# Performance work log

Hardware: AMD Instinct MI355X
Metric: run time of the kernel (lower is better)

The kernel has to match this reference:

```python
import jax, jax.numpy as jnp
import numpy as np

# dims
B, N, D, H, S, LT, DE = 16, 32, 64, 8, 8, 128, 256  # B scenes, N trajs, d_in, heads, splits, seq, d_expand
L = LT // S
GROUPS = 8
EPS = 1e-5


def group_norm(x, gamma, beta):
    # x: (BN, C, L); normalize per group over (C//G, L)
    BN, C, Lx = x.shape
    xg = x.reshape(BN, GROUPS, (C // GROUPS) * Lx)
    mu = xg.mean(-1, keepdims=True)
    var = xg.var(-1, keepdims=True)
    xn = ((xg - mu) * jax.lax.rsqrt(var + EPS)).reshape(BN, C, Lx)
    return xn * gamma[None, :, None] + beta[None, :, None]


def conv1d(x, w, b, pad):
    # x: (BN, Cin, L), w: (Cout, Cin, K)
    y = jax.lax.conv_general_dilated(x, w, (1,), [(pad, pad)],
                                     dimension_numbers=('NCH', 'OIH', 'NCH'))
    return y + b[None, :, None]


def setup_inputs() -> dict:
    key = jax.random.key(0)
    ks = jax.random.split(key, 8)
    d_qkv = 3 * H * D
    sc = 0.02
    return {
        'x': jax.random.normal(ks[0], (B * N, D, LT), jnp.float32),
        'gn1_g': jnp.ones((D,), jnp.float32),
        'gn1_b': jnp.zeros((D,), jnp.float32),
        'w_qkv': sc * jax.random.normal(ks[1], (d_qkv, D, 3), jnp.float32),
        'b_qkv': jnp.zeros((d_qkv,), jnp.float32),
        'w_merge': sc * jax.random.normal(ks[2], (D, H * D, 3), jnp.float32),
        'b_merge': jnp.zeros((D,), jnp.float32),
        'gn2_g': jnp.ones((D,), jnp.float32),
        'gn2_b': jnp.zeros((D,), jnp.float32),
        'w_ff1': sc * jax.random.normal(ks[3], (DE, D, 3), jnp.float32),
        'b_ff1': jnp.zeros((DE,), jnp.float32),
        'w_ff2': sc * jax.random.normal(ks[4], (D, DE, 3), jnp.float32),
        'b_ff2': jnp.zeros((D,), jnp.float32),
    }


def reference(x, gn1_g, gn1_b, w_qkv, b_qkv, w_merge, b_merge,
              gn2_g, gn2_b, w_ff1, b_ff1, w_ff2, b_ff2):
    # QKV projection: GroupNorm + Conv1d(k=3,p=1)
    qkv = conv1d(group_norm(x, gn1_g, gn1_b), w_qkv, b_qkv, 1)  # (B*N, 3*H*D, LT)
    # rearrange '(B N) (T H C) (L S) -> T (B H) (N S) (C L)'
    qkv = qkv.reshape(B, N, 3, H, D, L, S).transpose(2, 0, 3, 1, 6, 4, 5)
    qkv = qkv.reshape(3, B * H, N * S, D * L)
    q, k, v = qkv[0], qkv[1], qkv[2]
    # attn = 1 / cdist(q, k, p=2)  (dropout is identity in eval mode)
    sq = ((q * q).sum(-1)[:, :, None] + (k * k).sum(-1)[:, None, :]
          - 2.0 * jnp.einsum('bid,bjd->bij', q, k))
    dist = jnp.sqrt(jnp.maximum(sq, 1e-12))
    attn = 1.0 / dist
    out = jnp.einsum('bij,bjd->bid', attn, v)  # (B*H, N*S, D*L)
    # rearrange '(B H) (N S) (C L) -> (B N) (H C) (L S)'
    out = out.reshape(B, H, N, S, D, L).transpose(0, 2, 1, 4, 5, 3)
    out = out.reshape(B * N, H * D, LT)
    x = x + conv1d(out, w_merge, b_merge, 1)
    # FFN: GroupNorm -> Conv -> Swish -> Conv ; shortcut is Identity (d_in==d_out)
    h = conv1d(group_norm(x, gn2_g, gn2_b), w_ff1, b_ff1, 1)
    h = h * jax.nn.sigmoid(h)
    y = conv1d(h, w_ff2, b_ff2, 1)
    return y + x
```

## Files before the change

kernel.cpp:

```cpp
#include <hip/hip_runtime.h>
#include <hip/hip_bf16.h>

#define DEV __device__ __forceinline__

typedef __attribute__((ext_vector_type(8))) __bf16 bf16x8;
typedef __attribute__((ext_vector_type(4))) float f32x4;

DEV float bfu(unsigned short u) { return __uint_as_float((unsigned int)u << 16); }
DEV unsigned short f2bf(float f) {
    union { float f; unsigned int u; } cv; cv.f = f;
    unsigned int u = cv.u;
    unsigned int r = (u + 0x7fffu + ((u >> 16) & 1u)) >> 16;
    return (unsigned short)r;
}
DEV unsigned int pack2(float a, float b) {
    return (unsigned int)f2bf(a) | ((unsigned int)f2bf(b) << 16);
}


__global__ __launch_bounds__(256) void gnstats_kernel(const float* __restrict__ src,
    const float* __restrict__ gamma, const float* __restrict__ beta,
    float* __restrict__ sa, float* __restrict__ sb)
{
    __shared__ float gsum[8], gsq[8];
    const int s = blockIdx.x, tid = threadIdx.x;
    const int g = tid >> 5, il = tid & 31;
    const float* p = src + (size_t)s * 8192 + g * 1024 + il;
    float sm = 0.f, sq = 0.f;
    #pragma unroll
    for (int m = 0; m < 32; ++m) {
        float v = p[m * 32];
        sm += v; sq += v * v;
    }
    #pragma unroll
    for (int m = 16; m; m >>= 1) { sm += __shfl_xor(sm, m); sq += __shfl_xor(sq, m); }
    if (il == 0) { gsum[g] = sm; gsq[g] = sq; }
    __syncthreads();
    if (tid < 64) {
        int gg = tid >> 3;
        float mu = gsum[gg] * (1.f / 1024.f);
        float var = gsq[gg] * (1.f / 1024.f) - mu * mu;
        float a = gamma[tid] * rsqrtf(var + 1e-5f);
        sa[s * 64 + tid] = a;
        sb[s * 64 + tid] = beta[tid] - mu * a;
    }
}

__global__ __launch_bounds__(256) void xprep_kernel(const float* __restrict__ src,
    const float* __restrict__ sa, const float* __restrict__ sb,
    unsigned short* __restrict__ xnt)
{
    __shared__ __align__(16) float sx[64][133];
    __shared__ float la[64], lb[64];
    const int s = blockIdx.x, tid = threadIdx.x;
    if (tid < 64) { la[tid] = sa[s * 64 + tid]; lb[tid] = sb[s * 64 + tid]; }
    for (int idx = tid; idx < 8192; idx += 256) {
        int c = idx >> 7, lt = idx & 127;
        sx[c][lt] = src[(size_t)s * 8192 + idx];
    }
    __syncthreads();
    for (int idx = tid; idx < 8320; idx += 256) {
        int row = idx >> 6, c = idx & 63;
        float v = 0.f;
        if (row >= 1 && row <= 128) v = sx[c][row - 1] * la[c] + lb[c];
        xnt[(size_t)s * 8320 + idx] = f2bf(v);
    }
}

__global__ __launch_bounds__(256) void prep_w_kernel(const float* __restrict__ w,
    unsigned short* __restrict__ dst, int n)
{
    int i = blockIdx.x * 256 + threadIdx.x;
    if (i < n) {
        #pragma unroll
        for (int k = 0; k < 3; ++k)
            dst[k * n + i] = f2bf(w[(size_t)i * 3 + k]);
    }
}

__global__ __launch_bounds__(256, 3) void conv_qkv_mfma(
    const unsigned short* __restrict__ xnt,
    const unsigned short* __restrict__ wq, const float* __restrict__ bias,
    unsigned short* __restrict__ qb, unsigned short* __restrict__ kb,
    unsigned short* __restrict__ vb, float* __restrict__ nq, float* __restrict__ nk,
    int b0)
{
    __shared__ __align__(16) char smem[34816];
    unsigned short (*xt)[72]  = (unsigned short(*)[72])smem;
    unsigned short (*ct)[136] = (unsigned short(*)[136])smem;

    const int mc = blockIdx.x, sl = blockIdx.y, tid = threadIdx.x;
    const int bn = b0 * 32 + sl;
    const int w = tid >> 6, lane = tid & 63;
    const int lrow = lane & 15, lko = (lane >> 4) * 8, q4 = lane >> 4;

    bf16x8 af[3][2][2];
    #pragma unroll
    for (int k = 0; k < 3; ++k)
        #pragma unroll
        for (int kc = 0; kc < 2; ++kc)
            #pragma unroll
            for (int m = 0; m < 2; ++m)
                af[k][kc][m] = *(const bf16x8*)(wq + (size_t)k * 98304 +
                    (size_t)(mc * 128 + w * 32 + m * 16 + lrow) * 64 + kc * 32 + lko);

    for (int idx = tid; idx < 1040; idx += 256)
        *(uint4*)&xt[idx >> 3][(idx & 7) * 8] = *(const uint4*)(xnt + (size_t)bn * 8320 + idx * 8);
    __syncthreads();

    f32x4 acc[2][8];
    #pragma unroll
    for (int m = 0; m < 2; ++m)
        #pragma unroll
        for (int n = 0; n < 8; ++n) acc[m][n] = (f32x4)0.f;
    #pragma unroll
    for (int k = 0; k < 3; ++k) {
        #pragma unroll
        for (int kc = 0; kc < 2; ++kc) {
            #pragma unroll
            for (int n = 0; n < 8; ++n) {
                bf16x8 b = *(const bf16x8*)&xt[n * 16 + lrow + k][kc * 32 + lko];
                acc[0][n] = __builtin_amdgcn_mfma_f32_16x16x32_bf16(af[k][kc][0], b, acc[0][n], 0, 0, 0);
                acc[1][n] = __builtin_amdgcn_mfma_f32_16x16x32_bf16(af[k][kc][1], b, acc[1][n], 0, 0, 0);
            }
        }
    }
    __syncthreads();
    const int c0 = mc * 128;
    float bv[2][4];
    #pragma unroll
    for (int m = 0; m < 2; ++m)
        #pragma unroll
        for (int r = 0; r < 4; ++r)
            bv[m][r] = bias[c0 + w * 32 + m * 16 + q4 * 4 + r];
    #pragma unroll
    for (int m = 0; m < 2; ++m)
        #pragma unroll
        for (int n = 0; n < 8; ++n)
            #pragma unroll
            for (int r = 0; r < 4; ++r)
                ct[w * 32 + m * 16 + q4 * 4 + r][n * 16 + lrow] =
                    f2bf(acc[m][n][r] + bv[m][r]);
    __syncthreads();
    const int t = mc >> 2, h_base = (mc & 3) * 2;
    const int bl = sl >> 5, n_tr = sl & 31;
    if (t < 2) {
        unsigned short* dst = t ? kb : qb;
        for (int idx = tid; idx < 2048; idx += 256) {
            int lb = idx & 1;
            int d  = (idx >> 1) & 63;
            int s  = (idx >> 7) & 7;
            int hl = idx >> 10;
            unsigned int uu[4];
            #pragma unroll
            for (int e2 = 0; e2 < 4; ++e2) {
                unsigned short w0 = ct[hl * 64 + d][(lb * 8 + e2 * 2) * 8 + s];
                unsigned short w1 = ct[hl * 64 + d][(lb * 8 + e2 * 2 + 1) * 8 + s];
                uu[e2] = (unsigned int)w0 | ((unsigned int)w1 << 16);
            }
            uint4 o = {uu[0], uu[1], uu[2], uu[3]};
            size_t a = ((size_t)((bl * 8 + h_base + hl) * 256 + n_tr * 8 + s)) * 1024 + d * 16 + lb * 8;
            *(uint4*)(dst + a) = o;
        }
        float* ndst = t ? nk : nq;
        const int tk = tid >> 4, l = tid & 15;
        const int hl = tk >> 3, sS = tk & 7;
        float s2 = 0.f;
        for (int d = 0; d < 64; ++d) {
            float v = bfu(ct[hl * 64 + d][l * 8 + sS]);
            s2 = fmaf(v, v, s2);
        }
        #pragma unroll
        for (int m = 8; m; m >>= 1) s2 += __shfl_xor(s2, m);
        if (l == 0)
            ndst[(bl * 8 + h_base + hl) * 256 + n_tr * 8 + sS] = s2;
    } else {
        for (int idx = tid; idx < 2048; idx += 256) {
            int l = idx & 15, d = (idx >> 4) & 63, hl = idx >> 10;
            uint4 o = *(const uint4*)&ct[hl * 64 + d][l * 8];
            size_t a = ((size_t)((bl * 8 + h_base + hl) * 1024 + d * 16 + l)) * 256 + n_tr * 8;
            *(uint4*)(vb + a) = o;
        }
    }
}

__global__ __launch_bounds__(256) void attnw_mfma(const unsigned short* __restrict__ qb,
    const unsigned short* __restrict__ kb, const float* __restrict__ nq,
    const float* __restrict__ nk, unsigned short* __restrict__ attn)
{
    __shared__ __align__(16) unsigned short q_s[128][136];
    __shared__ __align__(16) unsigned short k_s[128][136];
    const int bh = blockIdx.z, i0 = blockIdx.y * 128, j0 = blockIdx.x * 128;
    const int tid = threadIdx.x, w = tid >> 6, lane = tid & 63;
    const int wi = w >> 1, wj = w & 1;
    const int lrow = lane & 15, lko = (lane >> 4) * 8;
    f32x4 acc[4][4];
    #pragma unroll
    for (int m = 0; m < 4; ++m)
        #pragma unroll
        for (int n = 0; n < 4; ++n) acc[m][n] = (f32x4)0.f;
    const size_t tb = (size_t)bh * 262144;
    for (int fc = 0; fc < 8; ++fc) {
        __syncthreads();
        for (int idx = tid; idx < 2048; idx += 256) {
            int r = idx >> 4, c8 = (idx & 15) * 8;
            *(uint4*)&q_s[r][c8] = *(const uint4*)(qb + tb + (size_t)(i0 + r) * 1024 + fc * 128 + c8);
            *(uint4*)&k_s[r][c8] = *(const uint4*)(kb + tb + (size_t)(j0 + r) * 1024 + fc * 128 + c8);
        }
        __syncthreads();
        #pragma unroll
        for (int ks = 0; ks < 4; ++ks) {
            bf16x8 a[4], b[4];
            #pragma unroll
            for (int m = 0; m < 4; ++m) a[m] = *(const bf16x8*)&q_s[wi * 64 + m * 16 + lrow][ks * 32 + lko];
            #pragma unroll
            for (int n = 0; n < 4; ++n) b[n] = *(const bf16x8*)&k_s[wj * 64 + n * 16 + lrow][ks * 32 + lko];
            #pragma unroll
            for (int m = 0; m < 4; ++m)
                #pragma unroll
                for (int n = 0; n < 4; ++n)
                    acc[m][n] = __builtin_amdgcn_mfma_f32_16x16x32_bf16(a[m], b[n], acc[m][n], 0, 0, 0);
        }
    }
    float nqv[4][4], nkv[4];
    #pragma unroll
    for (int m = 0; m < 4; ++m)
        #pragma unroll
        for (int r = 0; r < 4; ++r)
            nqv[m][r] = nq[bh * 256 + i0 + wi * 64 + m * 16 + (lane >> 4) * 4 + r];
    #pragma unroll
    for (int n = 0; n < 4; ++n)
        nkv[n] = nk[bh * 256 + j0 + wj * 64 + n * 16 + lrow];
    __syncthreads();
    #pragma unroll
    for (int m = 0; m < 4; ++m)
        #pragma unroll
        for (int n = 0; n < 4; ++n)
            #pragma unroll
            for (int r = 0; r < 4; ++r) {
                float sq = nqv[m][r] + nkv[n] - 2.f * acc[m][n][r];
                q_s[wi * 64 + m * 16 + (lane >> 4) * 4 + r][wj * 64 + n * 16 + lrow] =
                    f2bf(rsqrtf(fmaxf(sq, 1e-12f)));
            }
    __syncthreads();
    for (int idx = tid; idx < 2048; idx += 256) {
        int r = idx >> 4, c8 = (idx & 15) * 8;
        *(uint4*)(attn + (size_t)bh * 65536 + (size_t)(i0 + r) * 256 + j0 + c8) =
            *(const uint4*)&q_s[r][c8];
    }
}

__global__ __launch_bounds__(256) void pv_mfma(const unsigned short* __restrict__ attn,
    const unsigned short* __restrict__ vb, unsigned short* __restrict__ umat)
{
    __shared__ __align__(16) unsigned short a_s[128][136];
    __shared__ __align__(16) unsigned short b_s[128][136];
    const int bh = blockIdx.z, i0 = blockIdx.y * 128, f0 = blockIdx.x * 128;
    const int tid = threadIdx.x, w = tid >> 6, lane = tid & 63;
    const int wi = w >> 1, wf = w & 1;
    const int lrow = lane & 15, lko = (lane >> 4) * 8;
    f32x4 acc[4][4];
    #pragma unroll
    for (int m = 0; m < 4; ++m)
        #pragma unroll
        for (int n = 0; n < 4; ++n) acc[m][n] = (f32x4)0.f;
    for (int jc = 0; jc < 2; ++jc) {
        __syncthreads();
        for (int idx = tid; idx < 2048; idx += 256) {
            int r = idx >> 4, c8 = (idx & 15) * 8;
            *(uint4*)&a_s[r][c8] = *(const uint4*)(attn + (size_t)bh * 65536 + (size_t)(i0 + r) * 256 + jc * 128 + c8);
            *(uint4*)&b_s[r][c8] = *(const uint4*)(vb + (size_t)bh * 262144 + (size_t)(f0 + r) * 256 + jc * 128 + c8);
        }
        __syncthreads();
        #pragma unroll
        for (int ks = 0; ks < 4; ++ks) {
            bf16x8 a[4], b[4];
            #pragma unroll
            for (int m = 0; m < 4; ++m) a[m] = *(const bf16x8*)&a_s[wi * 64 + m * 16 + lrow][ks * 32 + lko];
            #pragma unroll
            for (int n = 0; n < 4; ++n) b[n] = *(const bf16x8*)&b_s[wf * 64 + n * 16 + lrow][ks * 32 + lko];
            #pragma unroll
            for (int m = 0; m < 4; ++m)
                #pragma unroll
                for (int n = 0; n < 4; ++n)
                    acc[m][n] = __builtin_amdgcn_mfma_f32_16x16x32_bf16(a[m], b[n], acc[m][n], 0, 0, 0);
        }
    }
    __syncthreads();
    #pragma unroll
    for (int m = 0; m < 4; ++m)
        #pragma unroll
        for (int n = 0; n < 4; ++n)
            #pragma unroll
            for (int r = 0; r < 4; ++r)
                a_s[wi * 64 + m * 16 + (lane >> 4) * 4 + r][wf * 64 + n * 16 + lrow] = f2bf(acc[m][n][r]);
    __syncthreads();
    const int bl = bh >> 3, h = bh & 7;
    const int cinb = h * 64 + (f0 >> 4);
    for (int idx = tid; idx < 2048; idx += 256) {
        int r = idx >> 4;
        int l = idx & 15;
        int i = i0 + r;
        int nn = i >> 3, s = i & 7;
        int lt = l * 8 + s;
        unsigned int uu[4];
        #pragma unroll
        for (int e = 0; e < 4; ++e) {
            unsigned short w0 = a_s[r][(e * 2 + 0) * 16 + l];
            unsigned short w1 = a_s[r][(e * 2 + 1) * 16 + l];
            uu[e] = (unsigned int)w0 | ((unsigned int)w1 << 16);
        }
        uint4 o = {uu[0], uu[1], uu[2], uu[3]};
        *(uint4*)(umat + ((size_t)(bl * 32 + nn) * 128 + lt) * 512 + cinb) = o;
    }
}

__global__ __launch_bounds__(256, 3) void merge_mfma(const unsigned short* __restrict__ umat,
    const float* __restrict__ x, const unsigned short* __restrict__ wmg,
    const float* __restrict__ bias, float* __restrict__ x2, int b0)
{
    __shared__ __align__(16) unsigned short ut[130][136];
    const int sl = blockIdx.x, tid = threadIdx.x;
    const int bn = b0 * 32 + sl;
    const int w = tid >> 6, lane = tid & 63;
    const int lrow = lane & 15, lko = (lane >> 4) * 8, q4 = lane >> 4;
    if (tid < 128) { ut[0][tid] = 0; ut[129][tid] = 0; }
    f32x4 acc[2][4];
    #pragma unroll
    for (int m = 0; m < 2; ++m)
        #pragma unroll
        for (int n = 0; n < 4; ++n) acc[m][n] = (f32x4)0.f;
    for (int c4 = 0; c4 < 4; ++c4) {
        __syncthreads();
        for (int idx = tid; idx < 2048; idx += 256) {
            int lt = idx >> 4, ci8 = (idx & 15) * 8;
            *(uint4*)&ut[1 + lt][ci8] =
                *(const uint4*)(umat + ((size_t)sl * 128 + lt) * 512 + c4 * 128 + ci8);
        }
        bf16x8 af[3][4][2];
        #pragma unroll
        for (int k = 0; k < 3; ++k)
            #pragma unroll
            for (int kc = 0; kc < 4; ++kc)
                #pragma unroll
                for (int m = 0; m < 2; ++m)
                    af[k][kc][m] = *(const bf16x8*)(wmg + (size_t)k * 32768 +
                        (size_t)((w >> 1) * 32 + m * 16 + lrow) * 512 + c4 * 128 + kc * 32 + lko);
        __syncthreads();
        #pragma unroll
        for (int k = 0; k < 3; ++k) {
            #pragma unroll
            for (int kc = 0; kc < 4; ++kc) {
                bf16x8 b[4];
                #pragma unroll
                for (int n = 0; n < 4; ++n)
                    b[n] = *(const bf16x8*)&ut[(w & 1) * 64 + n * 16 + lrow + k][kc * 32 + lko];
                #pragma unroll
                for (int m = 0; m < 2; ++m)
                    #pragma unroll
                    for (int n = 0; n < 4; ++n)
                        acc[m][n] = __builtin_amdgcn_mfma_f32_16x16x32_bf16(af[k][kc][m], b[n], acc[m][n], 0, 0, 0);
            }
        }
    }
    #pragma unroll
    for (int m = 0; m < 2; ++m) {
        int cb = (w >> 1) * 32 + m * 16 + q4 * 4;
        float bv[4];
        #pragma unroll
        for (int r = 0; r < 4; ++r) bv[r] = bias[cb + r];
        #pragma unroll
        for (int n = 0; n < 4; ++n) {
            int lt = (w & 1) * 64 + n * 16 + lrow;
            #pragma unroll
            for (int r = 0; r < 4; ++r) {
                size_t a = (size_t)bn * 8192 + (size_t)(cb + r) * 128 + lt;
                x2[a] = acc[m][n][r] + bv[r] + x[a];
            }
        }
    }
}

__global__ __launch_bounds__(256, 3) void ff1_mfma(const unsigned short* __restrict__ xnt,
    const unsigned short* __restrict__ wf1, const float* __restrict__ bias,
    unsigned short* __restrict__ hb)
{
    __shared__ __align__(16) unsigned short xt[130][72];
    const int mc = blockIdx.x, bn = blockIdx.y, tid = threadIdx.x;
    const int w = tid >> 6, lane = tid & 63;
    const int lrow = lane & 15, lko = (lane >> 4) * 8, q4 = lane >> 4;
    bf16x8 af[3][2][2];
    #pragma unroll
    for (int k = 0; k < 3; ++k)
        #pragma unroll
        for (int kc = 0; kc < 2; ++kc)
            #pragma unroll
            for (int m = 0; m < 2; ++m)
                af[k][kc][m] = *(const bf16x8*)(wf1 + (size_t)k * 16384 +
                    (size_t)(mc * 128 + w * 32 + m * 16 + lrow) * 64 + kc * 32 + lko);
    for (int idx = tid; idx < 1040; idx += 256)
        *(uint4*)&xt[idx >> 3][(idx & 7) * 8] = *(const uint4*)(xnt + (size_t)bn * 8320 + idx * 8);
    __syncthreads();
    f32x4 acc[2][8];
    #pragma unroll
    for (int m = 0; m < 2; ++m)
        #pragma unroll
        for (int n = 0; n < 8; ++n) acc[m][n] = (f32x4)0.f;
    #pragma unroll
    for (int k = 0; k < 3; ++k) {
        #pragma unroll
        for (int kc = 0; kc < 2; ++kc) {
            #pragma unroll
            for (int n = 0; n < 8; ++n) {
                bf16x8 b = *(const bf16x8*)&xt[n * 16 + lrow + k][kc * 32 + lko];
                acc[0][n] = __builtin_amdgcn_mfma_f32_16x16x32_bf16(af[k][kc][0], b, acc[0][n], 0, 0, 0);
                acc[1][n] = __builtin_amdgcn_mfma_f32_16x16x32_bf16(af[k][kc][1], b, acc[1][n], 0, 0, 0);
            }
        }
    }
    #pragma unroll
    for (int m = 0; m < 2; ++m) {
        int rb = w * 32 + m * 16 + q4 * 4;
        float bv[4];
        #pragma unroll
        for (int r = 0; r < 4; ++r) bv[r] = bias[mc * 128 + rb + r];
        #pragma unroll
        for (int n = 0; n < 8; ++n) {
            int lt = n * 16 + lrow;
            float sws[4];
            #pragma unroll
            for (int r = 0; r < 4; ++r) {
                float t = acc[m][n][r] + bv[r];
                sws[r] = t / (1.f + __expf(-t));
            }
            uint2 o = {pack2(sws[0], sws[1]), pack2(sws[2], sws[3])};
            *(uint2*)(hb + (size_t)bn * 32768 + (size_t)lt * 256 + mc * 128 + rb) = o;
        }
    }
}

__global__ __launch_bounds__(256, 3) void ff2_mfma(const unsigned short* __restrict__ hb,
    const float* __restrict__ x2, const unsigned short* __restrict__ wf2,
    const float* __restrict__ bias, float* __restrict__ y)
{
    __shared__ __align__(16) unsigned short ut[130][136];
    const int bn = blockIdx.x, tid = threadIdx.x;
    const int w = tid >> 6, lane = tid & 63;
    const int lrow = lane & 15, lko = (lane >> 4) * 8, q4 = lane >> 4;
    if (tid < 128) { ut[0][tid] = 0; ut[129][tid] = 0; }
    f32x4 acc[2][4];
    #pragma unroll
    for (int m = 0; m < 2; ++m)
        #pragma unroll
        for (int n = 0; n < 4; ++n) acc[m][n] = (f32x4)0.f;
    for (int c2 = 0; c2 < 2; ++c2) {
        __syncthreads();
        for (int idx = tid; idx < 2048; idx += 256) {
            int lt = idx >> 4, ci8 = (idx & 15) * 8;
            *(uint4*)&ut[1 + lt][ci8] =
                *(const uint4*)(hb + (size_t)bn * 32768 + (size_t)lt * 256 + c2 * 128 + ci8);
        }
        bf16x8 af[3][4][2];
        #pragma unroll
        for (int k = 0; k < 3; ++k)
            #pragma unroll
            for (int kc = 0; kc < 4; ++kc)
                #pragma unroll
                for (int m = 0; m < 2; ++m)
                    af[k][kc][m] = *(const bf16x8*)(wf2 + (size_t)k * 16384 +
                        (size_t)((w >> 1) * 32 + m * 16 + lrow) * 256 + c2 * 128 + kc * 32 + lko);
        __syncthreads();
        #pragma unroll
        for (int k = 0; k < 3; ++k) {
            #pragma unroll
            for (int kc = 0; kc < 4; ++kc) {
                bf16x8 b[4];
                #pragma unroll
                for (int n = 0; n < 4; ++n)
                    b[n] = *(const bf16x8*)&ut[(w & 1) * 64 + n * 16 + lrow + k][kc * 32 + lko];
                #pragma unroll
                for (int m = 0; m < 2; ++m)
                    #pragma unroll
                    for (int n = 0; n < 4; ++n)
                        acc[m][n] = __builtin_amdgcn_mfma_f32_16x16x32_bf16(af[k][kc][m], b[n], acc[m][n], 0, 0, 0);
            }
        }
    }
    #pragma unroll
    for (int m = 0; m < 2; ++m) {
        int cb = (w >> 1) * 32 + m * 16 + q4 * 4;
        float bv[4];
        #pragma unroll
        for (int r = 0; r < 4; ++r) bv[r] = bias[cb + r];
        #pragma unroll
        for (int n = 0; n < 4; ++n) {
            int lt = (w & 1) * 64 + n * 16 + lrow;
            #pragma unroll
            for (int r = 0; r < 4; ++r) {
                size_t a = (size_t)bn * 8192 + (size_t)(cb + r) * 128 + lt;
                y[a] = acc[m][n][r] + bv[r] + x2[a];
            }
        }
    }
}

extern "C" void kernel_launch(void* const* d_in, const int* in_sizes, int n_in,
                              void* d_out, int out_size, void* d_ws, size_t ws_size,
                              hipStream_t stream) {
    (void)in_sizes; (void)n_in; (void)out_size;
    const float* x     = (const float*)d_in[0];
    const float* gn1_g = (const float*)d_in[1];
    const float* gn1_b = (const float*)d_in[2];
    const float* w_qkv = (const float*)d_in[3];
    const float* b_qkv = (const float*)d_in[4];
    const float* w_mg  = (const float*)d_in[5];
    const float* b_mg  = (const float*)d_in[6];
    const float* gn2_g = (const float*)d_in[7];
    const float* gn2_b = (const float*)d_in[8];
    const float* w_f1  = (const float*)d_in[9];
    const float* b_f1  = (const float*)d_in[10];
    const float* w_f2  = (const float*)d_in[11];
    const float* b_f2  = (const float*)d_in[12];
    float* y = (float*)d_out;

    char* ws = (char*)d_ws;
    const size_t OFF_SA1 = 0;
    const size_t OFF_SB1 = 131072;
    const size_t OFF_SA2 = 262144;
    const size_t OFF_SB2 = 393216;
    const size_t OFF_NQ  = 524288;
    const size_t OFF_NK  = 655360;
    const size_t OFF_WQ  = 786432;
    const size_t OFF_WMG = 1376256;
    const size_t OFF_WF1 = 1572864;
    const size_t OFF_WF2 = 1671168;
    const size_t OFF_X2  = 2097152;
    const size_t OFF_XNT = 18874368;
    const size_t OFF_CHUNK = 27394048;
    const size_t H_BYTES = 33554432;

    int CH = 1;
    {
        const int cands[5] = {16, 8, 4, 2, 1};
        for (int ci = 0; ci < 5; ++ci) {
            int c = cands[ci];
            size_t qsz = (size_t)c * 4194304;
            size_t asz = (size_t)c * 1048576;
            size_t body = 3 * qsz + asz;
            if (body < H_BYTES) body = H_BYTES;
            if (OFF_CHUNK + body <= ws_size) { CH = c; break; }
        }
    }
    const size_t QSZ = (size_t)CH * 4194304;
    const size_t OFF_Q    = OFF_CHUNK;
    const size_t OFF_K    = OFF_Q + QSZ;
    const size_t OFF_V    = OFF_K + QSZ;
    const size_t OFF_ATTN = OFF_V + QSZ;

    float* sa1 = (float*)(ws + OFF_SA1);
    float* sb1 = (float*)(ws + OFF_SB1);
    float* sa2 = (float*)(ws + OFF_SA2);
    float* sb2 = (float*)(ws + OFF_SB2);
    float* nqp = (float*)(ws + OFF_NQ);
    float* nkp = (float*)(ws + OFF_NK);
    unsigned short* wqb  = (unsigned short*)(ws + OFF_WQ);
    unsigned short* wmgb = (unsigned short*)(ws + OFF_WMG);
    unsigned short* wf1b = (unsigned short*)(ws + OFF_WF1);
    unsigned short* wf2b = (unsigned short*)(ws + OFF_WF2);
    float* x2  = (float*)(ws + OFF_X2);
    unsigned short* xnt  = (unsigned short*)(ws + OFF_XNT);
    unsigned short* qb   = (unsigned short*)(ws + OFF_Q);
    unsigned short* kb   = (unsigned short*)(ws + OFF_K);
    unsigned short* vbuf = (unsigned short*)(ws + OFF_V);
    unsigned short* attn = (unsigned short*)(ws + OFF_ATTN);
    unsigned short* umat = (unsigned short*)(ws + OFF_Q);
    unsigned short* hbuf = (unsigned short*)(ws + OFF_CHUNK);

    gnstats_kernel<<<512, 256, 0, stream>>>(x, gn1_g, gn1_b, sa1, sb1);
    xprep_kernel<<<512, 256, 0, stream>>>(x, sa1, sb1, xnt);
    prep_w_kernel<<<384, 256, 0, stream>>>(w_qkv, wqb, 98304);
    prep_w_kernel<<<128, 256, 0, stream>>>(w_mg,  wmgb, 32768);
    prep_w_kernel<<<64,  256, 0, stream>>>(w_f1,  wf1b, 16384);
    prep_w_kernel<<<64,  256, 0, stream>>>(w_f2,  wf2b, 16384);
    const int nch = 16 / CH;
    for (int cidx = 0; cidx < nch; ++cidx) {
        int b0 = cidx * CH;
        conv_qkv_mfma<<<dim3(12, CH * 32), 256, 0, stream>>>(xnt, wqb, b_qkv, qb, kb, vbuf, nqp, nkp, b0);
        attnw_mfma<<<dim3(2, 2, CH * 8), 256, 0, stream>>>(qb, kb, nqp, nkp, attn);
        pv_mfma<<<dim3(8, 2, CH * 8), 256, 0, stream>>>(attn, vbuf, umat);
        merge_mfma<<<CH * 32, 256, 0, stream>>>(umat, x, wmgb, b_mg, x2, b0);
    }
    gnstats_kernel<<<512, 256, 0, stream>>>(x2, gn2_g, gn2_b, sa2, sb2);
    xprep_kernel<<<512, 256, 0, stream>>>(x2, sa2, sb2, xnt);
    ff1_mfma<<<dim3(2, 512), 256, 0, stream>>>(xnt, wf1b, b_f1, hbuf);
    ff2_mfma<<<512, 256, 0, stream>>>(hbuf, x2, wf2b, b_f2, y);
}
```

Measured before the change: 329.4 us.

## Fuse attention weight and PV matmuls into one kernel, add V transpose pass

Replaces the separate attention-weight kernel and PV kernel with a single fused kernel. Each block computes a 128x256 inverse-distance tile kept in shared memory, then multiplies it by V directly, so the attention matrix never goes to global memory. V is now written in the Q/K layout by the conv kernel and transposed by a new vtrans kernel. The fused kernel uses about 134KB of shared memory and launches only 2 x CH*8 blocks, so parallelism and occupancy are much lower.

```diff
diff --git a/kernel.cpp b/kernel.cpp
--- a/kernel.cpp
+++ b/kernel.cpp
@@ -82,7 +82,7 @@
     const unsigned short* __restrict__ xnt,
     const unsigned short* __restrict__ wq, const float* __restrict__ bias,
     unsigned short* __restrict__ qb, unsigned short* __restrict__ kb,
-    unsigned short* __restrict__ vb, float* __restrict__ nq, float* __restrict__ nk,
+    unsigned short* __restrict__ vt, float* __restrict__ nq, float* __restrict__ nk,
     int b0)
 {
     __shared__ __align__(16) char smem[34816];
@@ -144,24 +144,24 @@
     __syncthreads();
     const int t = mc >> 2, h_base = (mc & 3) * 2;
     const int bl = sl >> 5, n_tr = sl & 31;
+    unsigned short* dst = (t == 0) ? qb : ((t == 1) ? kb : vt);
+    for (int idx = tid; idx < 2048; idx += 256) {
+        int lb = idx & 1;
+        int d  = (idx >> 1) & 63;
+        int s  = (idx >> 7) & 7;
+        int hl = idx >> 10;
+        unsigned int uu[4];
+        #pragma unroll
+        for (int e2 = 0; e2 < 4; ++e2) {
+            unsigned short w0 = ct[hl * 64 + d][(lb * 8 + e2 * 2) * 8 + s];
+            unsigned short w1 = ct[hl * 64 + d][(lb * 8 + e2 * 2 + 1) * 8 + s];
+            uu[e2] = (unsigned int)w0 | ((unsigned int)w1 << 16);
+        }
+        uint4 o = {uu[0], uu[1], uu[2], uu[3]};
+        size_t a = ((size_t)((bl * 8 + h_base + hl) * 256 + n_tr * 8 + s)) * 1024 + d * 16 + lb * 8;
+        *(uint4*)(dst + a) = o;
+    }
     if (t < 2) {
-        unsigned short* dst = t ? kb : qb;
-        for (int idx = tid; idx < 2048; idx += 256) {
-            int lb = idx & 1;
-            int d  = (idx >> 1) & 63;
-            int s  = (idx >> 7) & 7;
-            int hl = idx >> 10;
-            unsigned int uu[4];
-            #pragma unroll
-            for (int e2 = 0; e2 < 4; ++e2) {
-                unsigned short w0 = ct[hl * 64 + d][(lb * 8 + e2 * 2) * 8 + s];
-                unsigned short w1 = ct[hl * 64 + d][(lb * 8 + e2 * 2 + 1) * 8 + s];
-                uu[e2] = (unsigned int)w0 | ((unsigned int)w1 << 16);
-            }
-            uint4 o = {uu[0], uu[1], uu[2], uu[3]};
-            size_t a = ((size_t)((bl * 8 + h_base + hl) * 256 + n_tr * 8 + s)) * 1024 + d * 16 + lb * 8;
-            *(uint4*)(dst + a) = o;
-        }
         float* ndst = t ? nk : nq;
         const int tk = tid >> 4, l = tid & 15;
         const int hl = tk >> 3, sS = tk & 7;
@@ -174,144 +174,165 @@
         for (int m = 8; m; m >>= 1) s2 += __shfl_xor(s2, m);
         if (l == 0)
             ndst[(bl * 8 + h_base + hl) * 256 + n_tr * 8 + sS] = s2;
-    } else {
-        for (int idx = tid; idx < 2048; idx += 256) {
-            int l = idx & 15, d = (idx >> 4) & 63, hl = idx >> 10;
-            uint4 o = *(const uint4*)&ct[hl * 64 + d][l * 8];
-            size_t a = ((size_t)((bl * 8 + h_base + hl) * 1024 + d * 16 + l)) * 256 + n_tr * 8;
-            *(uint4*)(vb + a) = o;
-        }
-    }
-}
-
-__global__ __launch_bounds__(256) void attnw_mfma(const unsigned short* __restrict__ qb,
+    }
+}
+
+__global__ __launch_bounds__(256) void vtrans_kernel(const unsigned short* __restrict__ vt,
+    unsigned short* __restrict__ vf)
+{
+    __shared__ __align__(16) unsigned short t_s[64][72];
+    const int dt = blockIdx.x, nt = blockIdx.y, bh = blockIdx.z, tid = threadIdx.x;
+    const size_t tb = (size_t)bh * 262144;
+    for (int idx = tid; idx < 512; idx += 256) {
+        int ns_l = idx >> 3, c8 = idx & 7;
+        int col = c8 ^ (ns_l >> 3);
+        *(uint4*)&t_s[ns_l][col * 8] =
+            *(const uint4*)(vt + tb + (size_t)(nt * 64 + ns_l) * 1024 + dt * 64 + c8 * 8);
+    }
+    __syncthreads();
+    for (int idx = tid; idx < 512; idx += 256) {
+        int dl_l = idx >> 3, nsb = idx & 7;
+        unsigned int uu[4];
+        #pragma unroll
+        for (int e2 = 0; e2 < 4; ++e2) {
+            int ns0 = nsb * 8 + e2 * 2, ns1 = ns0 + 1;
+            int cb = (dl_l >> 3) ^ nsb;
+            unsigned short w0 = t_s[ns0][cb * 8 + (dl_l & 7)];
+            unsigned short w1 = t_s[ns1][cb * 8 + (dl_l & 7)];
+            uu[e2] = (unsigned int)w0 | ((unsigned int)w1 << 16);
+        }
+        uint4 o = {uu[0], uu[1], uu[2], uu[3]};
+        *(uint4*)(vf + tb + (size_t)(dt * 64 + dl_l) * 256 + nt * 64 + nsb * 8) = o;
+    }
+}
+
+__global__ __launch_bounds__(256, 1) void attn_fused(const unsigned short* __restrict__ qb,
     const unsigned short* __restrict__ kb, const float* __restrict__ nq,
-    const float* __restrict__ nk, unsigned short* __restrict__ attn)
-{
-    __shared__ __align__(16) unsigned short q_s[128][136];
-    __shared__ __align__(16) unsigned short k_s[128][136];
-    const int bh = blockIdx.z, i0 = blockIdx.y * 128, j0 = blockIdx.x * 128;
-    const int tid = threadIdx.x, w = tid >> 6, lane = tid & 63;
+    const float* __restrict__ nk, const unsigned short* __restrict__ vf,
+    unsigned short* __restrict__ umat)
+{
+    __shared__ __align__(16) char smem[137216];
+    unsigned short (*Wm)[264] = (unsigned short(*)[264])smem;
+    unsigned short (*q_s)[136] = (unsigned short(*)[136])(smem + 67584);
+    unsigned short (*k_s)[136] = q_s + 128;
+    unsigned short (*b_s)[136] = q_s;
+    unsigned short (*ct)[264]  = (unsigned short(*)[264])(smem + 67584);
+
+    const int i0 = blockIdx.x, bh = blockIdx.y, tid = threadIdx.x;
+    const int w = tid >> 6, lane = tid & 63;
+    const int lrow = lane & 15, lko = (lane >> 4) * 8, q4 = lane >> 4;
+    const size_t tb = (size_t)bh * 262144;
+
     const int wi = w >> 1, wj = w & 1;
-    const int lrow = lane & 15, lko = (lane >> 4) * 8;
-    f32x4 acc[4][4];
+    float nqv[4][4];
     #pragma unroll
     for (int m = 0; m < 4; ++m)
         #pragma unroll
-        for (int n = 0; n < 4; ++n) acc[m][n] = (f32x4)0.f;
-    const size_t tb = (size_t)bh * 262144;
-    for (int fc = 0; fc < 8; ++fc) {
+        for (int r = 0; r < 4; ++r)
+            nqv[m][r] = nq[bh * 256 + i0 * 128 + wi * 64 + m * 16 + q4 * 4 + r];
+    for (int jh = 0; jh < 2; ++jh) {
+        f32x4 acc[4][4];
+        #pragma unroll
+        for (int m = 0; m < 4; ++m)
+            #pragma unroll
+            for (int n = 0; n < 4; ++n) acc[m][n] = (f32x4)0.f;
+        for (int fc = 0; fc < 8; ++fc) {
+            __syncthreads();
+            for (int idx = tid; idx < 2048; idx += 256) {
+                int r = idx >> 4, c8 = (idx & 15) * 8;
+                *(uint4*)&q_s[r][c8] = *(const uint4*)(qb + tb + (size_t)(i0 * 128 + r) * 1024 + fc * 128 + c8);
+                *(uint4*)&k_s[r][c8] = *(const uint4*)(kb + tb + (size_t)(jh * 128 + r) * 1024 + fc * 128 + c8);
+            }
+            __syncthreads();
+            #pragma unroll
+            for (int ks = 0; ks < 4; ++ks) {
+                bf16x8 a[4], b[4];
+                #pragma unroll
+                for (int m = 0; m < 4; ++m) a[m] = *(const bf16x8*)&q_s[wi * 64 + m * 16 + lrow][ks * 32 + lko];
+                #pragma unroll
+                for (int n = 0; n < 4; ++n) b[n] = *(const bf16x8*)&k_s[wj * 64 + n * 16 + lrow][ks * 32 + lko];
+                #pragma unroll
+                for (int m = 0; m < 4; ++m)
+                    #pragma unroll
+                    for (int n = 0; n < 4; ++n)
+                        acc[m][n] = __builtin_amdgcn_mfma_f32_16x16x32_bf16(a[m], b[n], acc[m][n], 0, 0, 0);
+            }
+        }
+        float nkv[4];
+        #pragma unroll
+        for (int n = 0; n < 4; ++n)
+            nkv[n] = nk[bh * 256 + jh * 128 + wj * 64 + n * 16 + lrow];
+        #pragma unroll
+        for (int m = 0; m < 4; ++m)
+            #pragma unroll
+            for (int n = 0; n < 4; ++n)
+                #pragma unroll
+                for (int r = 0; r < 4; ++r) {
+                    float sq = nqv[m][r] + nkv[n] - 2.f * acc[m][n][r];
+                    Wm[wi * 64 + m * 16 + q4 * 4 + r][jh * 128 + wj * 64 + n * 16 + lrow] =
+                        f2bf(rsqrtf(fmaxf(sq, 1e-12f)));
+                }
+    }
+
+    const int wi2 = w >> 1, wf2 = w & 1;
+    const int bl = bh >> 3, h = bh & 7;
+    for (int ch = 0; ch < 4; ++ch) {
+        f32x4 acc2[4][8];
+        #pragma unroll
+        for (int m = 0; m < 4; ++m)
+            #pragma unroll
+            for (int n = 0; n < 8; ++n) acc2[m][n] = (f32x4)0.f;
+        for (int jc = 0; jc < 2; ++jc) {
+            __syncthreads();
+            for (int idx = tid; idx < 4096; idx += 256) {
+                int fl = idx >> 4, j8 = (idx & 15) * 8;
+                *(uint4*)&b_s[fl][j8] =
+                    *(const uint4*)(vf + tb + (size_t)(ch * 256 + fl) * 256 + jc * 128 + j8);
+            }
+            __syncthreads();
+            #pragma unroll
+            for (int ks = 0; ks < 4; ++ks) {
+                bf16x8 a[4], b[8];
+                #pragma unroll
+                for (int m = 0; m < 4; ++m)
+                    a[m] = *(const bf16x8*)&Wm[wi2 * 64 + m * 16 + lrow][jc * 128 + ks * 32 + lko];
+                #pragma unroll
+                for (int n = 0; n < 8; ++n)
+                    b[n] = *(const bf16x8*)&b_s[wf2 * 128 + n * 16 + lrow][ks * 32 + lko];
+                #pragma unroll
+                for (int m = 0; m < 4; ++m)
+                    #pragma unroll
+                    for (int n = 0; n < 8; ++n)
+                        acc2[m][n] = __builtin_amdgcn_mfma_f32_16x16x32_bf16(a[m], b[n], acc2[m][n], 0, 0, 0);
+            }
+        }
+        __syncthreads();
+        #pragma unroll
+        for (int m = 0; m < 4; ++m)
+            #pragma unroll
+            for (int n = 0; n < 8; ++n)
+                #pragma unroll
+                for (int r = 0; r < 4; ++r)
+                    ct[wi2 * 64 + m * 16 + q4 * 4 + r][wf2 * 128 + n * 16 + lrow] = f2bf(acc2[m][n][r]);
         __syncthreads();
         for (int idx = tid; idx < 2048; idx += 256) {
-            int r = idx >> 4, c8 = (idx & 15) * 8;
-            *(uint4*)&q_s[r][c8] = *(const uint4*)(qb + tb + (size_t)(i0 + r) * 1024 + fc * 128 + c8);
-            *(uint4*)&k_s[r][c8] = *(const uint4*)(kb + tb + (size_t)(j0 + r) * 1024 + fc * 128 + c8);
-        }
-        __syncthreads();
-        #pragma unroll
-        for (int ks = 0; ks < 4; ++ks) {
-            bf16x8 a[4], b[4];
-            #pragma unroll
-            for (int m = 0; m < 4; ++m) a[m] = *(const bf16x8*)&q_s[wi * 64 + m * 16 + lrow][ks * 32 + lko];
-            #pragma unroll
-            for (int n = 0; n < 4; ++n) b[n] = *(const bf16x8*)&k_s[wj * 64 + n * 16 + lrow][ks * 32 + lko];
-            #pragma unroll
-            for (int m = 0; m < 4; ++m)
-                #pragma unroll
-                for (int n = 0; n < 4; ++n)
-                    acc[m][n] = __builtin_amdgcn_mfma_f32_16x16x32_bf16(a[m], b[n], acc[m][n], 0, 0, 0);
-        }
-    }
-    float nqv[4][4], nkv[4];
-    #pragma unroll
-    for (int m = 0; m < 4; ++m)
-        #pragma unroll
-        for (int r = 0; r < 4; ++r)
-            nqv[m][r] = nq[bh * 256 + i0 + wi * 64 + m * 16 + (lane >> 4) * 4 + r];
-    #pragma unroll
-    for (int n = 0; n < 4; ++n)
-        nkv[n] = nk[bh * 256 + j0 + wj * 64 + n * 16 + lrow];
-    __syncthreads();
-    #pragma unroll
-    for (int m = 0; m < 4; ++m)
-        #pragma unroll
-        for (int n = 0; n < 4; ++n)
-            #pragma unroll
-            for (int r = 0; r < 4; ++r) {
-                float sq = nqv[m][r] + nkv[n] - 2.f * acc[m][n][r];
-                q_s[wi * 64 + m * 16 + (lane >> 4) * 4 + r][wj * 64 + n * 16 + lrow] =
-                    f2bf(rsqrtf(fmaxf(sq, 1e-12f)));
-            }
-    __syncthreads();
-    for (int idx = tid; idx < 2048; idx += 256) {
-        int r = idx >> 4, c8 = (idx & 15) * 8;
-        *(uint4*)(attn + (size_t)bh * 65536 + (size_t)(i0 + r) * 256 + j0 + c8) =
-            *(const uint4*)&q_s[r][c8];
-    }
-}
-
-__global__ __launch_bounds__(256) void pv_mfma(const unsigned short* __restrict__ attn,
-    const unsigned short* __restrict__ vb, unsigned short* __restrict__ umat)
-{
-    __shared__ __align__(16) unsigned short a_s[128][136];
-    __shared__ __align__(16) unsigned short b_s[128][136];
-    const int bh = blockIdx.z, i0 = blockIdx.y * 128, f0 = blockIdx.x * 128;
-    const int tid = threadIdx.x, w = tid >> 6, lane = tid & 63;
-    const int wi = w >> 1, wf = w & 1;
-    const int lrow = lane & 15, lko = (lane >> 4) * 8;
-    f32x4 acc[4][4];
-    #pragma unroll
-    for (int m = 0; m < 4; ++m)
-        #pragma unroll
-        for (int n = 0; n < 4; ++n) acc[m][n] = (f32x4)0.f;
-    for (int jc = 0; jc < 2; ++jc) {
-        __syncthreads();
-        for (int idx = tid; idx < 2048; idx += 256) {
-            int r = idx >> 4, c8 = (idx & 15) * 8;
-            *(uint4*)&a_s[r][c8] = *(const uint4*)(attn + (size_t)bh * 65536 + (size_t)(i0 + r) * 256 + jc * 128 + c8);
-            *(uint4*)&b_s[r][c8] = *(const uint4*)(vb + (size_t)bh * 262144 + (size_t)(f0 + r) * 256 + jc * 128 + c8);
-        }
-        __syncthreads();
-        #pragma unroll
-        for (int ks = 0; ks < 4; ++ks) {
-            bf16x8 a[4], b[4];
-            #pragma unroll
-            for (int m = 0; m < 4; ++m) a[m] = *(const bf16x8*)&a_s[wi * 64 + m * 16 + lrow][ks * 32 + lko];
-            #pragma unroll
-            for (int n = 0; n < 4; ++n) b[n] = *(const bf16x8*)&b_s[wf * 64 + n * 16 + lrow][ks * 32 + lko];
-            #pragma unroll
-            for (int m = 0; m < 4; ++m)
-                #pragma unroll
-                for (int n = 0; n < 4; ++n)
-                    acc[m][n] = __builtin_amdgcn_mfma_f32_16x16x32_bf16(a[m], b[n], acc[m][n], 0, 0, 0);
-        }
-    }
-    __syncthreads();
-    #pragma unroll
-    for (int m = 0; m < 4; ++m)
-        #pragma unroll
-        for (int n = 0; n < 4; ++n)
-            #pragma unroll
-            for (int r = 0; r < 4; ++r)
-                a_s[wi * 64 + m * 16 + (lane >> 4) * 4 + r][wf * 64 + n * 16 + lrow] = f2bf(acc[m][n][r]);
-    __syncthreads();
-    const int bl = bh >> 3, h = bh & 7;
-    const int cinb = h * 64 + (f0 >> 4);
-    for (int idx = tid; idx < 2048; idx += 256) {
-        int r = idx >> 4;
-        int l = idx & 15;
-        int i = i0 + r;
-        int nn = i >> 3, s = i & 7;
-        int lt = l * 8 + s;
-        unsigned int uu[4];
-        #pragma unroll
-        for (int e = 0; e < 4; ++e) {
-            unsigned short w0 = a_s[r][(e * 2 + 0) * 16 + l];
-            unsigned short w1 = a_s[r][(e * 2 + 1) * 16 + l];
-            uu[e] = (unsigned int)w0 | ((unsigned int)w1 << 16);
-        }
-        uint4 o = {uu[0], uu[1], uu[2], uu[3]};
-        *(uint4*)(umat + ((size_t)(bl * 32 + nn) * 128 + lt) * 512 + cinb) = o;
+            int i = idx >> 4, l = idx & 15;
+            int gi = i0 * 128 + i;
+            int nn = gi >> 3, s = gi & 7;
+            int lt = l * 8 + s;
+            unsigned int uu[8];
+            #pragma unroll
+            for (int e = 0; e < 8; ++e) {
+                unsigned short w0 = ct[i][(e * 2 + 0) * 16 + l];
+                unsigned short w1 = ct[i][(e * 2 + 1) * 16 + l];
+                uu[e] = (unsigned int)w0 | ((unsigned int)w1 << 16);
+            }
+            size_t base = ((size_t)(bl * 32 + nn) * 128 + lt) * 512 + h * 64 + ch * 16;
+            uint4 o0 = {uu[0], uu[1], uu[2], uu[3]};
+            uint4 o1 = {uu[4], uu[5], uu[6], uu[7]};
+            *(uint4*)(umat + base) = o0;
+            *(uint4*)(umat + base + 8) = o1;
+        }
     }
 }
 
@@ -545,17 +566,16 @@
         for (int ci = 0; ci < 5; ++ci) {
             int c = cands[ci];
             size_t qsz = (size_t)c * 4194304;
-            size_t asz = (size_t)c * 1048576;
-            size_t body = 3 * qsz + asz;
+            size_t body = 4 * qsz;
             if (body < H_BYTES) body = H_BYTES;
             if (OFF_CHUNK + body <= ws_size) { CH = c; break; }
         }
     }
     const size_t QSZ = (size_t)CH * 4194304;
-    const size_t OFF_Q    = OFF_CHUNK;
-    const size_t OFF_K    = OFF_Q + QSZ;
-    const size_t OFF_V    = OFF_K + QSZ;
-    const size_t OFF_ATTN = OFF_V + QSZ;
+    const size_t OFF_Q  = OFF_CHUNK;
+    const size_t OFF_K  = OFF_Q + QSZ;
+    const size_t OFF_VT = OFF_K + QSZ;
+    const size_t OFF_VF = OFF_VT + QSZ;
 
     float* sa1 = (float*)(ws + OFF_SA1);
     float* sb1 = (float*)(ws + OFF_SB1);
@@ -571,9 +591,9 @@
     unsigned short* xnt  = (unsigned short*)(ws + OFF_XNT);
     unsigned short* qb   = (unsigned short*)(ws + OFF_Q);
     unsigned short* kb   = (unsigned short*)(ws + OFF_K);
-    unsigned short* vbuf = (unsigned short*)(ws + OFF_V);
-    unsigned short* attn = (unsigned short*)(ws + OFF_ATTN);
-    unsigned short* umat = (unsigned short*)(ws + OFF_Q);
+    unsigned short* vtb  = (unsigned short*)(ws + OFF_VT);
+    unsigned short* vfb  = (unsigned short*)(ws + OFF_VF);
+    unsigned short* umat = (unsigned short*)(ws + OFF_VT);
     unsigned short* hbuf = (unsigned short*)(ws + OFF_CHUNK);
 
     gnstats_kernel<<<512, 256, 0, stream>>>(x, gn1_g, gn1_b, sa1, sb1);
@@ -585,9 +605,9 @@
     const int nch = 16 / CH;
     for (int cidx = 0; cidx < nch; ++cidx) {
         int b0 = cidx * CH;
-        conv_qkv_mfma<<<dim3(12, CH * 32), 256, 0, stream>>>(xnt, wqb, b_qkv, qb, kb, vbuf, nqp, nkp, b0);
-        attnw_mfma<<<dim3(2, 2, CH * 8), 256, 0, stream>>>(qb, kb, nqp, nkp, attn);
-        pv_mfma<<<dim3(8, 2, CH * 8), 256, 0, stream>>>(attn, vbuf, umat);
+        conv_qkv_mfma<<<dim3(12, CH * 32), 256, 0, stream>>>(xnt, wqb, b_qkv, qb, kb, vtb, nqp, nkp, b0);
+        vtrans_kernel<<<dim3(16, 4, CH * 8), 256, 0, stream>>>(vtb, vfb);
+        attn_fused<<<dim3(2, CH * 8), 256, 0, stream>>>(qb, kb, nqp, nkp, vfb, umat);
         merge_mfma<<<CH * 32, 256, 0, stream>>>(umat, x, wmgb, b_mg, x2, b0);
     }
     gnstats_kernel<<<512, 256, 0, stream>>>(x2, gn2_g, gn2_b, sa2, sb2);
```

Measured after the change: 489.2 us. 48.5% more time.

## Fuse GroupNorm stats with normalize pass and store V in Q/K layout

Applied to the files above, without the earlier changes.

The separate GroupNorm statistics and normalize/transpose kernels become one kernel that loads each slice into shared memory once, computes group statistics from shared memory and writes the bf16 padded transpose. This saves one global read of the activations and one launch, twice per call. The V output of the QKV conv now uses the same coalesced packed layout as Q and K. The PV kernel transposes V into shared memory with scalar 16-bit stores, which adds LDS write traffic and possible bank conflicts in exchange for cheaper global writes in the conv.

```diff
diff --git a/kernel.cpp b/kernel.cpp
--- a/kernel.cpp
+++ b/kernel.cpp
@@ -18,18 +18,24 @@
 }
 
 
-__global__ __launch_bounds__(256) void gnstats_kernel(const float* __restrict__ src,
+__global__ __launch_bounds__(256) void gnx_kernel(const float* __restrict__ src,
     const float* __restrict__ gamma, const float* __restrict__ beta,
-    float* __restrict__ sa, float* __restrict__ sb)
-{
-    __shared__ float gsum[8], gsq[8];
+    unsigned short* __restrict__ xnt)
+{
+    __shared__ __align__(16) float sx[64][133];
+    __shared__ float gsum[8], gsq[8], la[64], lb[64];
     const int s = blockIdx.x, tid = threadIdx.x;
+    for (int idx = tid; idx < 8192; idx += 256) {
+        int c = idx >> 7, lt = idx & 127;
+        sx[c][lt] = src[(size_t)s * 8192 + idx];
+    }
+    __syncthreads();
     const int g = tid >> 5, il = tid & 31;
-    const float* p = src + (size_t)s * 8192 + g * 1024 + il;
     float sm = 0.f, sq = 0.f;
     #pragma unroll
     for (int m = 0; m < 32; ++m) {
-        float v = p[m * 32];
+        int e = il + m * 32;
+        float v = sx[g * 8 + (e >> 7)][e & 127];
         sm += v; sq += v * v;
     }
     #pragma unroll
@@ -41,22 +47,7 @@
         float mu = gsum[gg] * (1.f / 1024.f);
         float var = gsq[gg] * (1.f / 1024.f) - mu * mu;
         float a = gamma[tid] * rsqrtf(var + 1e-5f);
-        sa[s * 64 + tid] = a;
-        sb[s * 64 + tid] = beta[tid] - mu * a;
-    }
-}
-
-__global__ __launch_bounds__(256) void xprep_kernel(const float* __restrict__ src,
-    const float* __restrict__ sa, const float* __restrict__ sb,
-    unsigned short* __restrict__ xnt)
-{
-    __shared__ __align__(16) float sx[64][133];
-    __shared__ float la[64], lb[64];
-    const int s = blockIdx.x, tid = threadIdx.x;
-    if (tid < 64) { la[tid] = sa[s * 64 + tid]; lb[tid] = sb[s * 64 + tid]; }
-    for (int idx = tid; idx < 8192; idx += 256) {
-        int c = idx >> 7, lt = idx & 127;
-        sx[c][lt] = src[(size_t)s * 8192 + idx];
+        la[tid] = a; lb[tid] = beta[tid] - mu * a;
     }
     __syncthreads();
     for (int idx = tid; idx < 8320; idx += 256) {
@@ -82,7 +73,7 @@
     const unsigned short* __restrict__ xnt,
     const unsigned short* __restrict__ wq, const float* __restrict__ bias,
     unsigned short* __restrict__ qb, unsigned short* __restrict__ kb,
-    unsigned short* __restrict__ vb, float* __restrict__ nq, float* __restrict__ nk,
+    unsigned short* __restrict__ vt, float* __restrict__ nq, float* __restrict__ nk,
     int b0)
 {
     __shared__ __align__(16) char smem[34816];
@@ -144,24 +135,24 @@
     __syncthreads();
     const int t = mc >> 2, h_base = (mc & 3) * 2;
     const int bl = sl >> 5, n_tr = sl & 31;
+    unsigned short* dst = (t == 0) ? qb : ((t == 1) ? kb : vt);
+    for (int idx = tid; idx < 2048; idx += 256) {
+        int lb = idx & 1;
+        int d  = (idx >> 1) & 63;
+        int s  = (idx >> 7) & 7;
+        int hl = idx >> 10;
+        unsigned int uu[4];
+        #pragma unroll
+        for (int e2 = 0; e2 < 4; ++e2) {
+            unsigned short w0 = ct[hl * 64 + d][(lb * 8 + e2 * 2) * 8 + s];
+            unsigned short w1 = ct[hl * 64 + d][(lb * 8 + e2 * 2 + 1) * 8 + s];
+            uu[e2] = (unsigned int)w0 | ((unsigned int)w1 << 16);
+        }
+        uint4 o = {uu[0], uu[1], uu[2], uu[3]};
+        size_t a = ((size_t)((bl * 8 + h_base + hl) * 256 + n_tr * 8 + s)) * 1024 + d * 16 + lb * 8;
+        *(uint4*)(dst + a) = o;
+    }
     if (t < 2) {
-        unsigned short* dst = t ? kb : qb;
-        for (int idx = tid; idx < 2048; idx += 256) {
-            int lb = idx & 1;
-            int d  = (idx >> 1) & 63;
-            int s  = (idx >> 7) & 7;
-            int hl = idx >> 10;
-            unsigned int uu[4];
-            #pragma unroll
-            for (int e2 = 0; e2 < 4; ++e2) {
-                unsigned short w0 = ct[hl * 64 + d][(lb * 8 + e2 * 2) * 8 + s];
-                unsigned short w1 = ct[hl * 64 + d][(lb * 8 + e2 * 2 + 1) * 8 + s];
-                uu[e2] = (unsigned int)w0 | ((unsigned int)w1 << 16);
-            }
-            uint4 o = {uu[0], uu[1], uu[2], uu[3]};
-            size_t a = ((size_t)((bl * 8 + h_base + hl) * 256 + n_tr * 8 + s)) * 1024 + d * 16 + lb * 8;
-            *(uint4*)(dst + a) = o;
-        }
         float* ndst = t ? nk : nq;
         const int tk = tid >> 4, l = tid & 15;
         const int hl = tk >> 3, sS = tk & 7;
@@ -174,13 +165,6 @@
         for (int m = 8; m; m >>= 1) s2 += __shfl_xor(s2, m);
         if (l == 0)
             ndst[(bl * 8 + h_base + hl) * 256 + n_tr * 8 + sS] = s2;
-    } else {
-        for (int idx = tid; idx < 2048; idx += 256) {
-            int l = idx & 15, d = (idx >> 4) & 63, hl = idx >> 10;
-            uint4 o = *(const uint4*)&ct[hl * 64 + d][l * 8];
-            size_t a = ((size_t)((bl * 8 + h_base + hl) * 1024 + d * 16 + l)) * 256 + n_tr * 8;
-            *(uint4*)(vb + a) = o;
-        }
     }
 }
 
@@ -250,8 +234,8 @@
     }
 }
 
-__global__ __launch_bounds__(256) void pv_mfma(const unsigned short* __restrict__ attn,
-    const unsigned short* __restrict__ vb, unsigned short* __restrict__ umat)
+__global__ __launch_bounds__(256) void pv_mfma_t(const unsigned short* __restrict__ attn,
+    const unsigned short* __restrict__ vt, unsigned short* __restrict__ umat)
 {
     __shared__ __align__(16) unsigned short a_s[128][136];
     __shared__ __align__(16) unsigned short b_s[128][136];
@@ -259,6 +243,7 @@
     const int tid = threadIdx.x, w = tid >> 6, lane = tid & 63;
     const int wi = w >> 1, wf = w & 1;
     const int lrow = lane & 15, lko = (lane >> 4) * 8;
+    const size_t tb = (size_t)bh * 262144;
     f32x4 acc[4][4];
     #pragma unroll
     for (int m = 0; m < 4; ++m)
@@ -269,7 +254,18 @@
         for (int idx = tid; idx < 2048; idx += 256) {
             int r = idx >> 4, c8 = (idx & 15) * 8;
             *(uint4*)&a_s[r][c8] = *(const uint4*)(attn + (size_t)bh * 65536 + (size_t)(i0 + r) * 256 + jc * 128 + c8);
-            *(uint4*)&b_s[r][c8] = *(const uint4*)(vb + (size_t)bh * 262144 + (size_t)(f0 + r) * 256 + jc * 128 + c8);
+        }
+        for (int idx = tid; idx < 2048; idx += 256) {
+            int j = idx & 127, fo = idx >> 7;
+            uint4 v = *(const uint4*)(vt + tb + (size_t)(jc * 128 + j) * 1024 + f0 + fo * 8);
+            b_s[fo * 8 + 0][j] = (unsigned short)(v.x);
+            b_s[fo * 8 + 1][j] = (unsigned short)(v.x >> 16);
+            b_s[fo * 8 + 2][j] = (unsigned short)(v.y);
+            b_s[fo * 8 + 3][j] = (unsigned short)(v.y >> 16);
+            b_s[fo * 8 + 4][j] = (unsigned short)(v.z);
+            b_s[fo * 8 + 5][j] = (unsigned short)(v.z >> 16);
+            b_s[fo * 8 + 6][j] = (unsigned short)(v.w);
+            b_s[fo * 8 + 7][j] = (unsigned short)(v.w >> 16);
         }
         __syncthreads();
         #pragma unroll
@@ -524,19 +520,15 @@
     float* y = (float*)d_out;
 
     char* ws = (char*)d_ws;
-    const size_t OFF_SA1 = 0;
-    const size_t OFF_SB1 = 131072;
-    const size_t OFF_SA2 = 262144;
-    const size_t OFF_SB2 = 393216;
-    const size_t OFF_NQ  = 524288;
-    const size_t OFF_NK  = 655360;
-    const size_t OFF_WQ  = 786432;
-    const size_t OFF_WMG = 1376256;
-    const size_t OFF_WF1 = 1572864;
-    const size_t OFF_WF2 = 1671168;
-    const size_t OFF_X2  = 2097152;
-    const size_t OFF_XNT = 18874368;
-    const size_t OFF_CHUNK = 27394048;
+    const size_t OFF_NQ  = 0;
+    const size_t OFF_NK  = 131072;
+    const size_t OFF_WQ  = 262144;
+    const size_t OFF_WMG = 917504;
+    const size_t OFF_WF1 = 1114112;
+    const size_t OFF_WF2 = 1212416;
+    const size_t OFF_X2  = 1310720;
+    const size_t OFF_XNT = 18087936;
+    const size_t OFF_CHUNK = 26607616;
     const size_t H_BYTES = 33554432;
 
     int CH = 1;
@@ -552,15 +544,11 @@
         }
     }
     const size_t QSZ = (size_t)CH * 4194304;
-    const size_t OFF_Q    = OFF_CHUNK;
-    const size_t OFF_K    = OFF_Q + QSZ;
-    const size_t OFF_V    = OFF_K + QSZ;
-    const size_t OFF_ATTN = OFF_V + QSZ;
-
-    float* sa1 = (float*)(ws + OFF_SA1);
-    float* sb1 = (float*)(ws + OFF_SB1);
-    float* sa2 = (float*)(ws + OFF_SA2);
-    float* sb2 = (float*)(ws + OFF_SB2);
+    const size_t OFF_Q  = OFF_CHUNK;
+    const size_t OFF_K  = OFF_Q + QSZ;
+    const size_t OFF_VT = OFF_K + QSZ;
+    const size_t OFF_AT = OFF_VT + QSZ;
+
     float* nqp = (float*)(ws + OFF_NQ);
     float* nkp = (float*)(ws + OFF_NK);
     unsigned short* wqb  = (unsigned short*)(ws + OFF_WQ);
@@ -571,13 +559,12 @@
     unsigned short* xnt  = (unsigned short*)(ws + OFF_XNT);
     unsigned short* qb   = (unsigned short*)(ws + OFF_Q);
     unsigned short* kb   = (unsigned short*)(ws + OFF_K);
-    unsigned short* vbuf = (unsigned short*)(ws + OFF_V);
-    unsigned short* attn = (unsigned short*)(ws + OFF_ATTN);
+    unsigned short* vtb  = (unsigned short*)(ws + OFF_VT);
+    unsigned short* attn = (unsigned short*)(ws + OFF_AT);
     unsigned short* umat = (unsigned short*)(ws + OFF_Q);
     unsigned short* hbuf = (unsigned short*)(ws + OFF_CHUNK);
 
-    gnstats_kernel<<<512, 256, 0, stream>>>(x, gn1_g, gn1_b, sa1, sb1);
-    xprep_kernel<<<512, 256, 0, stream>>>(x, sa1, sb1, xnt);
+    gnx_kernel<<<512, 256, 0, stream>>>(x, gn1_g, gn1_b, xnt);
     prep_w_kernel<<<384, 256, 0, stream>>>(w_qkv, wqb, 98304);
     prep_w_kernel<<<128, 256, 0, stream>>>(w_mg,  wmgb, 32768);
     prep_w_kernel<<<64,  256, 0, stream>>>(w_f1,  wf1b, 16384);
@@ -585,13 +572,12 @@
     const int nch = 16 / CH;
     for (int cidx = 0; cidx < nch; ++cidx) {
         int b0 = cidx * CH;
-        conv_qkv_mfma<<<dim3(12, CH * 32), 256, 0, stream>>>(xnt, wqb, b_qkv, qb, kb, vbuf, nqp, nkp, b0);
+        conv_qkv_mfma<<<dim3(12, CH * 32), 256, 0, stream>>>(xnt, wqb, b_qkv, qb, kb, vtb, nqp, nkp, b0);
         attnw_mfma<<<dim3(2, 2, CH * 8), 256, 0, stream>>>(qb, kb, nqp, nkp, attn);
-        pv_mfma<<<dim3(8, 2, CH * 8), 256, 0, stream>>>(attn, vbuf, umat);
+        pv_mfma_t<<<dim3(8, 2, CH * 8), 256, 0, stream>>>(attn, vtb, umat);
         merge_mfma<<<CH * 32, 256, 0, stream>>>(umat, x, wmgb, b_mg, x2, b0);
     }
-    gnstats_kernel<<<512, 256, 0, stream>>>(x2, gn2_g, gn2_b, sa2, sb2);
-    xprep_kernel<<<512, 256, 0, stream>>>(x2, sa2, sb2, xnt);
+    gnx_kernel<<<512, 256, 0, stream>>>(x2, gn2_g, gn2_b, xnt);
     ff1_mfma<<<dim3(2, 512), 256, 0, stream>>>(xnt, wf1b, b_f1, hbuf);
     ff2_mfma<<<512, 256, 0, stream>>>(hbuf, x2, wf2b, b_f2, y);
 }
```

After: 321.8 us. 2.3% less time.
